# Performance work log

Measured on AMD Instinct MI355X. Metric: run time of the kernel, lower is better.

The kernel has to match this reference:

```python
import jax, jax.numpy as jnp
import numpy as np

N_NODES = 50000
N_EDGES = 1600000
D = 128


def setup_inputs() -> dict:
    key = jax.random.key(0)
    k1, k2, k3, k4 = jax.random.split(key, 4)
    x = jax.random.normal(k1, (N_NODES, D), dtype=jnp.float32)
    edge_index = jax.random.randint(k2, (2, N_EDGES), 0, N_NODES, dtype=jnp.int64)
    # Xavier-uniform-like W; B is zeros in torch init but use small random for grad coverage
    limit = float(np.sqrt(6.0 / (D + D)))
    W = jax.random.uniform(k3, (D, D), dtype=jnp.float32, minval=-limit, maxval=limit)
    B = jax.random.uniform(k4, (D, D), dtype=jnp.float32, minval=-limit, maxval=limit)
    return {"x": x, "edge_index": edge_index, "W": W, "B": B}


def reference(x, edge_index, W, B):
    sources = edge_index[0]
    destinations = edge_index[1]
    # gather messages from source nodes, scatter-add into destinations
    messages = x[sources]  # [E, D]
    aggregated = jax.ops.segment_sum(messages, destinations, num_segments=N_NODES)  # [N, D]
    deg = jax.ops.segment_sum(jnp.ones((N_EDGES,), dtype=x.dtype), destinations, num_segments=N_NODES)
    deg = jnp.where(deg == 0, jnp.asarray(1.0, dtype=x.dtype), deg)
    mean_msg = aggregated / deg[:, None]
    # update: messages @ W.T + x @ B.T
    return mean_msg @ W.T + x @ B.T
```

## Files before the change

kernel.cpp:

```cpp
#include <hip/hip_runtime.h>
#include <hip/hip_bf16.h>

#define NN 50000
#define NE 1600000
#define DD 128
#define NPB 64
#define NBK 782
#define MAXB 2560
#define HSLAB 1280
#define CHUNK 3072
#define NCB 521
#define WS 136

typedef __attribute__((ext_vector_type(8))) short short8;
typedef __attribute__((ext_vector_type(4))) float f32x4;

__device__ inline unsigned short to_bf16(float v) {
    __hip_bfloat16 h = __float2bfloat16(v);
    return __builtin_bit_cast(unsigned short, h);
}
__device__ inline float bf2f(unsigned short u) {
    return __uint_as_float((unsigned)u << 16);
}

__global__ __launch_bounds__(1024) void convscatter_k(const int* __restrict__ ei,
                                                      const float* __restrict__ x,
                                                      const float* __restrict__ W,
                                                      const float* __restrict__ Bm,
                                                      unsigned int* __restrict__ xb,
                                                      unsigned short* __restrict__ Wbf,
                                                      unsigned short* __restrict__ Bbf,
                                                      int* __restrict__ gcursor,
                                                      int* __restrict__ ebuf) {
    __shared__ int stg[CHUNK];
    __shared__ int h[NBK];
    __shared__ int lbase[NBK];
    __shared__ int gb[NBK];
    __shared__ int hcur[NBK];
    __shared__ int wsum[16], wbase[16];
    const int t = threadIdx.x;
    const int lane = t & 63, wv = t >> 6;
    const int e0 = blockIdx.x * CHUNK;
    const int ec = min(CHUNK, NE - e0);

    for (int i = t; i < NBK; i += 1024) h[i] = 0;
    __syncthreads();

    unsigned int w2[3];
    #pragma unroll
    for (int u = 0; u < 3; ++u) {
        int i = u * 1024 + t;
        if (i < ec) {
            int src = ei[e0 + i];
            int dst = ei[NE + e0 + i];
            int b = dst >> 6;
            w2[u] = ((unsigned)b << 22) | ((unsigned)src << 6) | (unsigned)(dst & 63);
            atomicAdd(&h[b], 1);
        } else w2[u] = 0xFFFFFFFFu;
    }

    {
        int gid = blockIdx.x * 1024 + t;
        const int total4 = NN * DD / 4;
        for (int i = gid; i < total4; i += NCB * 1024) {
            float4 v = ((const float4*)x)[i];
            int p = __builtin_amdgcn_cvt_pk_fp8_f32(v.x, v.y, 0, false);
            p = __builtin_amdgcn_cvt_pk_fp8_f32(v.z, v.w, p, true);
            xb[i] = (unsigned)p;
        }
    }
    if (blockIdx.x == NCB - 1) {
        for (int i = t; i < DD * DD / 4; i += 1024) {
            float4 w4 = ((const float4*)W)[i];
            float4 b4 = ((const float4*)Bm)[i];
            ushort4 wp, bp;
            wp.x = to_bf16(w4.x); wp.y = to_bf16(w4.y); wp.z = to_bf16(w4.z); wp.w = to_bf16(w4.w);
            bp.x = to_bf16(b4.x); bp.y = to_bf16(b4.y); bp.z = to_bf16(b4.z); bp.w = to_bf16(b4.w);
            ((ushort4*)Wbf)[i] = wp;
            ((ushort4*)Bbf)[i] = bp;
        }
    }
    __syncthreads();

    int v = (t < NBK) ? h[t] : 0;
    int s = v;
    #pragma unroll
    for (int o = 1; o < 64; o <<= 1) {
        int u = __shfl_up(s, o);
        if (lane >= o) s += u;
    }
    if (lane == 63) wsum[wv] = s;
    __syncthreads();
    if (wv == 0 && lane < 16) {
        int bv = wsum[lane];
        int bs = bv;
        #pragma unroll
        for (int o = 1; o < 16; o <<= 1) {
            int u = __shfl_up(bs, o);
            if (lane >= o) bs += u;
        }
        wbase[lane] = bs - bv;
    }
    __syncthreads();
    if (t < NBK) {
        int excl = s - v + wbase[wv];
        lbase[t] = excl;
        hcur[t] = excl;
        gb[t] = v ? t * MAXB + atomicAdd(&gcursor[t], v) : 0;
    }
    __syncthreads();

    #pragma unroll
    for (int u = 0; u < 3; ++u) {
        if (w2[u] != 0xFFFFFFFFu) {
            int b = w2[u] >> 22;
            int pos = atomicAdd(&hcur[b], 1);
            stg[pos] = (int)w2[u];
        }
    }
    __syncthreads();

    for (int i = t; i < ec; i += 1024) {
        unsigned int w = (unsigned)stg[i];
        int b = w >> 22;
        ebuf[gb[b] + (i - lbase[b])] = (int)(w & 0x3FFFFFu);
    }
}

#define ACC2(U)                                                              \
    {                                                                        \
        auto l0 = __builtin_amdgcn_cvt_pk_f32_fp8((int)(U).x, false);        \
        auto h0 = __builtin_amdgcn_cvt_pk_f32_fp8((int)(U).x, true);         \
        auto l1 = __builtin_amdgcn_cvt_pk_f32_fp8((int)(U).y, false);        \
        auto h1 = __builtin_amdgcn_cvt_pk_f32_fp8((int)(U).y, true);         \
        a0 += l0[0]; a1 += l0[1]; a2 += h0[0]; a3 += h0[1];                  \
        a4 += l1[0]; a5 += l1[1]; a6 += h1[0]; a7 += h1[1];                  \
    }

__global__ __launch_bounds__(512) void sortagg_k(const unsigned int* __restrict__ xb,
                                                 const int* __restrict__ ebuf,
                                                 const int* __restrict__ gcursor,
                                                 unsigned short* __restrict__ psb,
                                                 unsigned short* __restrict__ pcnt) {
    __shared__ int stg[HSLAB];
    __shared__ unsigned short srt[HSLAB];
    __shared__ int cnt8[8][NPB];
    __shared__ int cur[NPB], off[NPB + 1];
    const int blk = blockIdx.x;
    const int b = blk >> 1, hb = blk & 1;
    const int t = threadIdx.x;
    const int wv = t >> 6, lane = t & 63;
    const int n = min(gcursor[b], MAXB);
    const int mid = n >> 1;
    const int g0 = hb ? mid : 0, g1 = hb ? n : mid;
    const int len = g1 - g0;
    const int* __restrict__ slab = ebuf + (size_t)b * MAXB + g0;

    cnt8[wv][lane] = 0;
    for (int i = t; i < len; i += 512) {
        int v = slab[i];
        stg[i] = v;
        atomicAdd(&cnt8[wv][v & 63], 1);
    }
    __syncthreads();
    if (t < 64) {
        int v = 0;
        #pragma unroll
        for (int w = 0; w < 8; ++w) v += cnt8[w][t];
        int s = v;
        #pragma unroll
        for (int o = 1; o < 64; o <<= 1) {
            int u = __shfl_up(s, o);
            if (t >= o) s += u;
        }
        cur[t] = s - v;
        off[t] = s - v;
        if (t == 63) off[64] = s;
    }
    __syncthreads();
    for (int i = t; i < len; i += 512) {
        int w = stg[i];
        int pos = atomicAdd(&cur[w & 63], 1);
        srt[pos] = (unsigned short)(w >> 6);
    }
    __syncthreads();

    const int sub = lane >> 4, il2 = lane & 15;
    #pragma unroll
    for (int q = 0; q < 8; ++q) {
        int ln = wv + q * 8;
        int s0 = off[ln], s1 = off[ln + 1];
        float a0 = 0.f, a1 = 0.f, a2 = 0.f, a3 = 0.f;
        float a4 = 0.f, a5 = 0.f, a6 = 0.f, a7 = 0.f;
        int i = s0;
        for (; i + 16 <= s1; i += 16) {
            uint2 u[4];
            #pragma unroll
            for (int k = 0; k < 4; ++k)
                u[k] = ((const uint2*)xb)[(size_t)srt[i + 4 * k + sub] * 16 + il2];
            #pragma unroll
            for (int k = 0; k < 4; ++k) ACC2(u[k]);
        }
        if (i < s1) {
            uint2 u[4];
            #pragma unroll
            for (int k = 0; k < 4; ++k) {
                int e = i + 4 * k + sub;
                if (e < s1) u[k] = ((const uint2*)xb)[(size_t)srt[e] * 16 + il2];
                else { u[k].x = 0u; u[k].y = 0u; }
            }
            #pragma unroll
            for (int k = 0; k < 4; ++k) ACC2(u[k]);
        }
        a0 += __shfl_xor(a0, 16); a0 += __shfl_xor(a0, 32);
        a1 += __shfl_xor(a1, 16); a1 += __shfl_xor(a1, 32);
        a2 += __shfl_xor(a2, 16); a2 += __shfl_xor(a2, 32);
        a3 += __shfl_xor(a3, 16); a3 += __shfl_xor(a3, 32);
        a4 += __shfl_xor(a4, 16); a4 += __shfl_xor(a4, 32);
        a5 += __shfl_xor(a5, 16); a5 += __shfl_xor(a5, 32);
        a6 += __shfl_xor(a6, 16); a6 += __shfl_xor(a6, 32);
        a7 += __shfl_xor(a7, 16); a7 += __shfl_xor(a7, 32);
        int node = b * NPB + ln;
        if (node < NN) {
            if (lane < 16) {
                short8 sv;
                sv[0] = (short)to_bf16(a0); sv[1] = (short)to_bf16(a1);
                sv[2] = (short)to_bf16(a2); sv[3] = (short)to_bf16(a3);
                sv[4] = (short)to_bf16(a4); sv[5] = (short)to_bf16(a5);
                sv[6] = (short)to_bf16(a6); sv[7] = (short)to_bf16(a7);
                *(short8*)&psb[((size_t)hb * NN + node) * DD + il2 * 8] = sv;
            }
            if (lane == 0) pcnt[hb * NN + node] = (unsigned short)(s1 - s0);
        }
    }
}

__global__ __launch_bounds__(512) void gemm_mfma_k(const unsigned short* __restrict__ psb,
                                                   const unsigned short* __restrict__ pcnt,
                                                   const float* __restrict__ x,
                                                   const unsigned short* __restrict__ Wbf,
                                                   const unsigned short* __restrict__ Bbf,
                                                   float* __restrict__ out) {
    __shared__ unsigned short Wt[DD * WS];
    __shared__ unsigned short Bt[DD * WS];
    const int tid = threadIdx.x;
    #pragma unroll
    for (int it = 0; it < 8; ++it) {
        int idx = it * 512 + tid;
        int n = idx >> 5;
        int k0 = (idx & 31) * 4;
        *(ushort4*)&Wt[n * WS + k0] = ((const ushort4*)Wbf)[idx];
        *(ushort4*)&Bt[n * WS + k0] = ((const ushort4*)Bbf)[idx];
    }
    __syncthreads();

    const int wave = tid >> 6;
    const int lane = tid & 63;
    const int m = lane & 15;
    const int quad = lane >> 4;
    const int rowA = min(blockIdx.x * 128 + wave * 16 + m, NN - 1);

    const float deg = (float)(pcnt[rowA] + pcnt[NN + rowA]);
    const float inv = 1.0f / fmaxf(deg, 1.0f);

    f32x4 acc[8];
    #pragma unroll
    for (int nt = 0; nt < 8; ++nt) acc[nt] = (f32x4){0.f, 0.f, 0.f, 0.f};

    #pragma unroll
    for (int t = 0; t < 4; ++t) {
        const int k8 = t * 32 + quad * 8;
        short8 p0 = *(const short8*)&psb[(size_t)rowA * DD + k8];
        short8 p1 = *(const short8*)&psb[((size_t)NN + rowA) * DD + k8];
        short8 mf;
        #pragma unroll
        for (int j = 0; j < 8; ++j) {
            float sm = bf2f((unsigned short)p0[j]) + bf2f((unsigned short)p1[j]);
            mf[j] = (short)to_bf16(sm * inv);
        }

        float xv[8];
        {
            const float4* xq = (const float4*)&x[(size_t)rowA * DD + k8];
            float4 b0 = xq[0], b1 = xq[1];
            xv[0] = b0.x; xv[1] = b0.y; xv[2] = b0.z; xv[3] = b0.w;
            xv[4] = b1.x; xv[5] = b1.y; xv[6] = b1.z; xv[7] = b1.w;
        }
        short8 xh, xl;
        #pragma unroll
        for (int j = 0; j < 8; ++j) {
            unsigned short g = to_bf16(xv[j]);
            xh[j] = (short)g;
            xl[j] = (short)to_bf16(xv[j] - __uint_as_float((unsigned)g << 16));
        }
        #pragma unroll
        for (int nt = 0; nt < 8; ++nt) {
            int nrow = nt * 16 + m;
            short8 wf = *(const short8*)&Wt[nrow * WS + k8];
            short8 bf = *(const short8*)&Bt[nrow * WS + k8];
            acc[nt] = __builtin_amdgcn_mfma_f32_16x16x32_bf16(xl, bf, acc[nt], 0, 0, 0);
            acc[nt] = __builtin_amdgcn_mfma_f32_16x16x32_bf16(mf, wf, acc[nt], 0, 0, 0);
            acc[nt] = __builtin_amdgcn_mfma_f32_16x16x32_bf16(xh, bf, acc[nt], 0, 0, 0);
        }
    }

    const int rowD0 = blockIdx.x * 128 + wave * 16 + quad * 4;
    #pragma unroll
    for (int nt = 0; nt < 8; ++nt) {
        #pragma unroll
        for (int r = 0; r < 4; ++r) {
            int row = rowD0 + r;
            if (row < NN) out[(size_t)row * DD + nt * 16 + m] = acc[nt][r];
        }
    }
}

extern "C" void kernel_launch(void* const* d_in, const int* in_sizes, int n_in,
                              void* d_out, int out_size, void* d_ws, size_t ws_size,
                              hipStream_t stream) {
    const float* x  = (const float*)d_in[0];
    const int*   ei = (const int*)d_in[1];
    const float* W  = (const float*)d_in[2];
    const float* Bm = (const float*)d_in[3];
    float* out = (float*)d_out;

    unsigned short* psb  = (unsigned short*)d_ws;
    unsigned int* xb     = (unsigned int*)(psb + 2 * (size_t)NN * DD);
    int* ebuf            = (int*)(xb + (size_t)NN * 32);
    unsigned short* Wbf  = (unsigned short*)(ebuf + (size_t)NBK * MAXB);
    unsigned short* Bbf  = Wbf + DD * DD;
    unsigned short* pcnt = Bbf + DD * DD;
    int* gcursor         = (int*)(pcnt + 2 * (size_t)NN);

    hipMemsetAsync(gcursor, 0, NBK * sizeof(int), stream);
    convscatter_k<<<NCB, 1024, 0, stream>>>(ei, x, W, Bm, xb, Wbf, Bbf, gcursor, ebuf);
    sortagg_k<<<NBK * 2, 512, 0, stream>>>(xb, ebuf, gcursor, psb, pcnt);
    gemm_mfma_k<<<(NN + 127) / 128, 512, 0, stream>>>(psb, pcnt, x, Wbf, Bbf, out);
}
```

Before: 155.3 us.

## Split each bucket's aggregation four ways and pad global cursors

Each destination bucket is now handled by four sortagg blocks instead of two. Every block works on a quarter slab and writes its own partial-sum plane, and the GEMM kernel adds four partial planes and four partial degree counts. The global cursor atomics are spaced 16 ints apart to avoid contention on shared cache lines, and they are issued earlier, before the prefix scan. This trades more parallelism and smaller shared-memory footprints for twice the partial-sum write/read traffic and bf16 partial storage.

```diff
diff --git a/kernel.cpp b/kernel.cpp
--- a/kernel.cpp
+++ b/kernel.cpp
@@ -7,10 +7,12 @@
 #define NPB 64
 #define NBK 782
 #define MAXB 2560
-#define HSLAB 1280
+#define QSLAB 640
+#define NSPL 4
 #define CHUNK 3072
 #define NCB 521
 #define WS 136
+#define GCS 16
 
 typedef __attribute__((ext_vector_type(8))) short short8;
 typedef __attribute__((ext_vector_type(4))) float f32x4;
@@ -83,6 +85,9 @@
     __syncthreads();
 
     int v = (t < NBK) ? h[t] : 0;
+    int gpos = 0;
+    if (v > 0) gpos = atomicAdd(&gcursor[t << 4], v);
+
     int s = v;
     #pragma unroll
     for (int o = 1; o < 64; o <<= 1) {
@@ -106,7 +111,7 @@
         int excl = s - v + wbase[wv];
         lbase[t] = excl;
         hcur[t] = excl;
-        gb[t] = v ? t * MAXB + atomicAdd(&gcursor[t], v) : 0;
+        gb[t] = v ? t * MAXB + gpos : 0;
     }
     __syncthreads();
 
@@ -142,17 +147,16 @@
                                                  const int* __restrict__ gcursor,
                                                  unsigned short* __restrict__ psb,
                                                  unsigned short* __restrict__ pcnt) {
-    __shared__ int stg[HSLAB];
-    __shared__ unsigned short srt[HSLAB];
+    __shared__ int stg[QSLAB];
+    __shared__ unsigned short srt[QSLAB];
     __shared__ int cnt8[8][NPB];
     __shared__ int cur[NPB], off[NPB + 1];
     const int blk = blockIdx.x;
-    const int b = blk >> 1, hb = blk & 1;
+    const int b = blk >> 2, hb = blk & 3;
     const int t = threadIdx.x;
     const int wv = t >> 6, lane = t & 63;
-    const int n = min(gcursor[b], MAXB);
-    const int mid = n >> 1;
-    const int g0 = hb ? mid : 0, g1 = hb ? n : mid;
+    const int n = min(gcursor[b << 4], MAXB);
+    const int g0 = (n * hb) >> 2, g1 = (n * (hb + 1)) >> 2;
     const int len = g1 - g0;
     const int* __restrict__ slab = ebuf + (size_t)b * MAXB + g0;
 
@@ -260,7 +264,8 @@
     const int quad = lane >> 4;
     const int rowA = min(blockIdx.x * 128 + wave * 16 + m, NN - 1);
 
-    const float deg = (float)(pcnt[rowA] + pcnt[NN + rowA]);
+    const float deg = (float)(pcnt[rowA] + pcnt[NN + rowA] +
+                              pcnt[2 * NN + rowA] + pcnt[3 * NN + rowA]);
     const float inv = 1.0f / fmaxf(deg, 1.0f);
 
     f32x4 acc[8];
@@ -272,10 +277,13 @@
         const int k8 = t * 32 + quad * 8;
         short8 p0 = *(const short8*)&psb[(size_t)rowA * DD + k8];
         short8 p1 = *(const short8*)&psb[((size_t)NN + rowA) * DD + k8];
+        short8 p2 = *(const short8*)&psb[((size_t)2 * NN + rowA) * DD + k8];
+        short8 p3 = *(const short8*)&psb[((size_t)3 * NN + rowA) * DD + k8];
         short8 mf;
         #pragma unroll
         for (int j = 0; j < 8; ++j) {
-            float sm = bf2f((unsigned short)p0[j]) + bf2f((unsigned short)p1[j]);
+            float sm = (bf2f((unsigned short)p0[j]) + bf2f((unsigned short)p1[j])) +
+                       (bf2f((unsigned short)p2[j]) + bf2f((unsigned short)p3[j]));
             mf[j] = (short)to_bf16(sm * inv);
         }
 
@@ -325,15 +333,15 @@
     float* out = (float*)d_out;
 
     unsigned short* psb  = (unsigned short*)d_ws;
-    unsigned int* xb     = (unsigned int*)(psb + 2 * (size_t)NN * DD);
+    unsigned int* xb     = (unsigned int*)(psb + (size_t)NSPL * NN * DD);
     int* ebuf            = (int*)(xb + (size_t)NN * 32);
     unsigned short* Wbf  = (unsigned short*)(ebuf + (size_t)NBK * MAXB);
     unsigned short* Bbf  = Wbf + DD * DD;
     unsigned short* pcnt = Bbf + DD * DD;
-    int* gcursor         = (int*)(pcnt + 2 * (size_t)NN);
-
-    hipMemsetAsync(gcursor, 0, NBK * sizeof(int), stream);
+    int* gcursor         = (int*)(pcnt + (size_t)NSPL * NN);
+
+    hipMemsetAsync(gcursor, 0, NBK * GCS * sizeof(int), stream);
     convscatter_k<<<NCB, 1024, 0, stream>>>(ei, x, W, Bm, xb, Wbf, Bbf, gcursor, ebuf);
-    sortagg_k<<<NBK * 2, 512, 0, stream>>>(xb, ebuf, gcursor, psb, pcnt);
+    sortagg_k<<<NBK * NSPL, 512, 0, stream>>>(xb, ebuf, gcursor, psb, pcnt);
     gemm_mfma_k<<<(NN + 127) / 128, 512, 0, stream>>>(psb, pcnt, x, Wbf, Bbf, out);
 }
```

Result: slower. 183.9 us (+18.4%).

## Aggregate each bucket in one 1024-thread block, removing split partial sums

Applied to the files above, without the earlier changes.

The sort-aggregate kernel now processes each 64-node bucket in a single 1024-thread block instead of two 512-thread half-blocks. Only one bf16 partial sum and one count per node are written, so the GEMM kernel reads half as much partial data and skips the add. The cost is fewer, larger blocks (782 instead of 1564) with more shared memory each, which may lower occupancy and load balance, and each wave now handles 4 nodes instead of 8.

```diff
diff --git a/kernel.cpp b/kernel.cpp
--- a/kernel.cpp
+++ b/kernel.cpp
@@ -7,7 +7,6 @@
 #define NPB 64
 #define NBK 782
 #define MAXB 2560
-#define HSLAB 1280
 #define CHUNK 3072
 #define NCB 521
 #define WS 136
@@ -137,36 +136,31 @@
         a4 += l1[0]; a5 += l1[1]; a6 += h1[0]; a7 += h1[1];                  \
     }
 
-__global__ __launch_bounds__(512) void sortagg_k(const unsigned int* __restrict__ xb,
-                                                 const int* __restrict__ ebuf,
-                                                 const int* __restrict__ gcursor,
-                                                 unsigned short* __restrict__ psb,
-                                                 unsigned short* __restrict__ pcnt) {
-    __shared__ int stg[HSLAB];
-    __shared__ unsigned short srt[HSLAB];
-    __shared__ int cnt8[8][NPB];
+__global__ __launch_bounds__(1024) void sortagg_k(const unsigned int* __restrict__ xb,
+                                                  const int* __restrict__ ebuf,
+                                                  const int* __restrict__ gcursor,
+                                                  unsigned short* __restrict__ psb,
+                                                  unsigned short* __restrict__ pcnt) {
+    __shared__ int stg[MAXB];
+    __shared__ unsigned short srt[MAXB];
+    __shared__ int cnt16[16][NPB];
     __shared__ int cur[NPB], off[NPB + 1];
-    const int blk = blockIdx.x;
-    const int b = blk >> 1, hb = blk & 1;
-    const int t = threadIdx.x;
+    const int b = blockIdx.x, t = threadIdx.x;
     const int wv = t >> 6, lane = t & 63;
     const int n = min(gcursor[b], MAXB);
-    const int mid = n >> 1;
-    const int g0 = hb ? mid : 0, g1 = hb ? n : mid;
-    const int len = g1 - g0;
-    const int* __restrict__ slab = ebuf + (size_t)b * MAXB + g0;
-
-    cnt8[wv][lane] = 0;
-    for (int i = t; i < len; i += 512) {
+    const int* __restrict__ slab = ebuf + (size_t)b * MAXB;
+
+    cnt16[wv][lane] = 0;
+    for (int i = t; i < n; i += 1024) {
         int v = slab[i];
         stg[i] = v;
-        atomicAdd(&cnt8[wv][v & 63], 1);
+        atomicAdd(&cnt16[wv][v & 63], 1);
     }
     __syncthreads();
     if (t < 64) {
         int v = 0;
         #pragma unroll
-        for (int w = 0; w < 8; ++w) v += cnt8[w][t];
+        for (int w = 0; w < 16; ++w) v += cnt16[w][t];
         int s = v;
         #pragma unroll
         for (int o = 1; o < 64; o <<= 1) {
@@ -178,7 +172,7 @@
         if (t == 63) off[64] = s;
     }
     __syncthreads();
-    for (int i = t; i < len; i += 512) {
+    for (int i = t; i < n; i += 1024) {
         int w = stg[i];
         int pos = atomicAdd(&cur[w & 63], 1);
         srt[pos] = (unsigned short)(w >> 6);
@@ -187,8 +181,8 @@
 
     const int sub = lane >> 4, il2 = lane & 15;
     #pragma unroll
-    for (int q = 0; q < 8; ++q) {
-        int ln = wv + q * 8;
+    for (int q = 0; q < 4; ++q) {
+        int ln = wv + q * 16;
         int s0 = off[ln], s1 = off[ln + 1];
         float a0 = 0.f, a1 = 0.f, a2 = 0.f, a3 = 0.f;
         float a4 = 0.f, a5 = 0.f, a6 = 0.f, a7 = 0.f;
@@ -228,9 +222,9 @@
                 sv[2] = (short)to_bf16(a2); sv[3] = (short)to_bf16(a3);
                 sv[4] = (short)to_bf16(a4); sv[5] = (short)to_bf16(a5);
                 sv[6] = (short)to_bf16(a6); sv[7] = (short)to_bf16(a7);
-                *(short8*)&psb[((size_t)hb * NN + node) * DD + il2 * 8] = sv;
+                *(short8*)&psb[(size_t)node * DD + il2 * 8] = sv;
             }
-            if (lane == 0) pcnt[hb * NN + node] = (unsigned short)(s1 - s0);
+            if (lane == 0) pcnt[node] = (unsigned short)(s1 - s0);
         }
     }
 }
@@ -260,7 +254,7 @@
     const int quad = lane >> 4;
     const int rowA = min(blockIdx.x * 128 + wave * 16 + m, NN - 1);
 
-    const float deg = (float)(pcnt[rowA] + pcnt[NN + rowA]);
+    const float deg = (float)pcnt[rowA];
     const float inv = 1.0f / fmaxf(deg, 1.0f);
 
     f32x4 acc[8];
@@ -271,13 +265,10 @@
     for (int t = 0; t < 4; ++t) {
         const int k8 = t * 32 + quad * 8;
         short8 p0 = *(const short8*)&psb[(size_t)rowA * DD + k8];
-        short8 p1 = *(const short8*)&psb[((size_t)NN + rowA) * DD + k8];
         short8 mf;
         #pragma unroll
-        for (int j = 0; j < 8; ++j) {
-            float sm = bf2f((unsigned short)p0[j]) + bf2f((unsigned short)p1[j]);
-            mf[j] = (short)to_bf16(sm * inv);
-        }
+        for (int j = 0; j < 8; ++j)
+            mf[j] = (short)to_bf16(bf2f((unsigned short)p0[j]) * inv);
 
         float xv[8];
         {
@@ -325,15 +316,15 @@
     float* out = (float*)d_out;
 
     unsigned short* psb  = (unsigned short*)d_ws;
-    unsigned int* xb     = (unsigned int*)(psb + 2 * (size_t)NN * DD);
+    unsigned int* xb     = (unsigned int*)(psb + (size_t)NN * DD);
     int* ebuf            = (int*)(xb + (size_t)NN * 32);
     unsigned short* Wbf  = (unsigned short*)(ebuf + (size_t)NBK * MAXB);
     unsigned short* Bbf  = Wbf + DD * DD;
     unsigned short* pcnt = Bbf + DD * DD;
-    int* gcursor         = (int*)(pcnt + 2 * (size_t)NN);
+    int* gcursor         = (int*)(pcnt + (size_t)NN + (NN & 1));
 
     hipMemsetAsync(gcursor, 0, NBK * sizeof(int), stream);
     convscatter_k<<<NCB, 1024, 0, stream>>>(ei, x, W, Bm, xb, Wbf, Bbf, gcursor, ebuf);
-    sortagg_k<<<NBK * 2, 512, 0, stream>>>(xb, ebuf, gcursor, psb, pcnt);
+    sortagg_k<<<NBK, 1024, 0, stream>>>(xb, ebuf, gcursor, psb, pcnt);
     gemm_mfma_k<<<(NN + 127) / 128, 512, 0, stream>>>(psb, pcnt, x, Wbf, Bbf, out);
 }
```

Result: no change. 154.4 us (-0.5%).
